# Kernel optimization log

Hardware: AMD Instinct MI355X
Metric: run time of the kernel (lower is better)

The kernel has to match this reference:

```python
import jax, jax.numpy as jnp
import numpy as np

C = 512
NUM_GROUPS = 4
EPS = 1e-6


def _conv1x1(W, b, t):
    # 1x1x1 Conv3d == per-position linear over channels
    return jnp.einsum('oc,bcfhw->bofhw', W, t) + b[None, :, None, None, None]


def setup_inputs() -> dict:
    key = jax.random.key(0)
    ks = jax.random.split(key, 11)
    c = C
    x = jax.random.normal(ks[0], (12, c, 48, 48), dtype=jnp.float32)
    p = lambda k: jax.random.normal(k, (c, c), dtype=jnp.float32) * 0.02
    return {
        'x': x,
        'norm_scale': jnp.ones((c,), jnp.float32),
        'norm_bias': jnp.zeros((c,), jnp.float32),
        'q_w': p(ks[1]), 'q_b': jnp.zeros((c,), jnp.float32),
        'k_w': p(ks[2]), 'k_b': jnp.zeros((c,), jnp.float32),
        'v_w': p(ks[3]), 'v_b': jnp.zeros((c,), jnp.float32),
        'proj_w': p(ks[4]), 'proj_b': jnp.zeros((c,), jnp.float32),
    }


def reference(x, norm_scale, norm_bias, q_w, q_b, k_w, k_b, v_w, v_b, proj_w, proj_b):
    b3, c, h, w = x.shape
    b = b3 // 3
    # chunk batch into 3 frames, stack at frame dim -> (b, c, 3, h, w)
    h_ = jnp.stack(jnp.split(x, 3, axis=0), axis=2)
    # GroupNorm(num_groups=4) over (C/G, F, H, W) per group
    g = NUM_GROUPS
    xg = h_.reshape(b, g, c // g, 3, h, w)
    mean = jnp.mean(xg, axis=(2, 3, 4, 5), keepdims=True)
    var = jnp.var(xg, axis=(2, 3, 4, 5), keepdims=True)
    xn = ((xg - mean) * jax.lax.rsqrt(var + EPS)).reshape(b, c, 3, h, w)
    hn = xn * norm_scale[None, :, None, None, None] + norm_bias[None, :, None, None, None]
    q = _conv1x1(q_w, q_b, hn)[:, :, 1:2]          # middle frame only: (b,c,1,h,w)
    skip = q[:, :, 0]                               # (b,c,h,w)
    k = _conv1x1(k_w, k_b, hn)                      # (b,c,3,h,w)
    v = _conv1x1(v_w, v_b, hn)
    n = h * w
    qf = q.reshape(b, c, n)                         # (b,c,n)
    kf = k.reshape(b, c, 3 * n)                     # (b,c,3n)
    vf = v.reshape(b, c, 3 * n)
    scores = jnp.einsum('bcn,bcm->bnm', qf, kf) * (float(c) ** -0.5)
    attn = jax.nn.softmax(scores, axis=2)           # (b,n,3n)
    out = jnp.einsum('bcm,bnm->bcn', vf, attn).reshape(b, c, 1, h, w)
    out = _conv1x1(proj_w, proj_b, out)[:, :, 0]
    return skip + out
```

## Files before the change

### kernel.cpp

```cpp
#include <hip/hip_runtime.h>

typedef unsigned short u16;
typedef unsigned long long u64;
typedef __attribute__((ext_vector_type(8))) short short8;
typedef __attribute__((ext_vector_type(4))) float f32x4;

__device__ __forceinline__ float bf2f(u16 h) {
    union { unsigned int u; float f; } v; v.u = ((unsigned int)h) << 16; return v.f;
}
__device__ __forceinline__ u16 f2bf(float f) {
    union { float f; unsigned int u; } v; v.f = f;
    unsigned int r = v.u + 0x7fffu + ((v.u >> 16) & 1u);
    return (u16)(r >> 16);
}

__device__ __forceinline__ void gload16(const u16* g, u16* l) {
    __builtin_amdgcn_global_load_lds(
        (const __attribute__((address_space(1))) void*)g,
        (__attribute__((address_space(3))) void*)l,
        16, 0, 0);
}

__device__ __forceinline__ float waveSum(float v) {
#pragma unroll
    for (int o = 32; o > 0; o >>= 1) v += __shfl_down(v, o);
    return v;
}
__device__ __forceinline__ float waveMax(float v) {
#pragma unroll
    for (int o = 32; o > 0; o >>= 1) v = fmaxf(v, __shfl_down(v, o));
    return v;
}
__device__ __forceinline__ int waveSumI(int v) {
#pragma unroll
    for (int o = 32; o > 0; o >>= 1) v += __shfl_down(v, o);
    return v;
}

__global__ __launch_bounds__(256) void detect_k(const u16* __restrict__ x, int* __restrict__ flag) {
    __shared__ int cnt[4];
    int c = 0;
    for (int i = threadIdx.x; i < 8192; i += 256) {
        u16 e = x[i * 2];
        int ex = (e >> 7) & 0xFF;
        c += (ex == 0 || (ex >= 100 && ex <= 150)) ? 1 : 0;
    }
    c = waveSumI(c);
    if ((threadIdx.x & 63) == 0) cnt[threadIdx.x >> 6] = c;
    __syncthreads();
    if (threadIdx.x == 0)
        flag[0] = ((cnt[0] + cnt[1] + cnt[2] + cnt[3]) > 4915) ? 1 : 0;
}

__global__ __launch_bounds__(256) void conv_k(const void* __restrict__ src, u16* __restrict__ dst,
                                              int n8, const int* __restrict__ flag) {
    int i = blockIdx.x * 256 + threadIdx.x;
    if (i >= n8) return;
    if (flag[0]) {
        ((int4*)dst)[i] = ((const int4*)src)[i];
    } else {
        const float* f = (const float*)src + (size_t)i * 8;
        union { int4 v4; u16 o[8]; } tv;
#pragma unroll
        for (int j = 0; j < 8; j++) tv.o[j] = f2bf(f[j]);
        ((int4*)dst)[i] = tv.v4;
    }
}

__global__ __launch_bounds__(256) void conv_w4(const void* s0, const void* s1, const void* s2, const void* s3,
                                               u16* __restrict__ dst, const int* __restrict__ flag) {
    int i = blockIdx.x * 256 + threadIdx.x;
    int w = blockIdx.y;
    const void* s = w == 0 ? s0 : w == 1 ? s1 : w == 2 ? s2 : s3;
    u16* d = dst + (size_t)w * 262144;
    if (flag[0]) {
        ((int4*)d)[i] = ((const int4*)s)[i];
    } else {
        const float* f = (const float*)s + (size_t)i * 8;
        union { int4 v4; u16 o[8]; } tv;
#pragma unroll
        for (int j = 0; j < 8; j++) tv.o[j] = f2bf(f[j]);
        ((int4*)d)[i] = tv.v4;
    }
}

__global__ __launch_bounds__(256) void conv_v6(const void* s0, const void* s1, const void* s2,
                                               const void* s3, const void* s4, const void* s5,
                                               u16* __restrict__ dst, const int* __restrict__ flag) {
    for (int i = threadIdx.x; i < 384; i += 256) {
        int seg = i >> 6, off = i & 63;
        const void* s = seg == 0 ? s0 : seg == 1 ? s1 : seg == 2 ? s2 : seg == 3 ? s3 : seg == 4 ? s4 : s5;
        u16* d = dst + (size_t)seg * 512;
        if (flag[0]) {
            ((int4*)d)[off] = ((const int4*)s)[off];
        } else {
            const float* f = (const float*)s + (size_t)off * 8;
            union { int4 v4; u16 o[8]; } tv;
#pragma unroll
            for (int j = 0; j < 8; j++) tv.o[j] = f2bf(f[j]);
            ((int4*)d)[off] = tv.v4;
        }
    }
}

__global__ __launch_bounds__(256) void gn_stats(const u16* __restrict__ x, float* __restrict__ stat) {
    __shared__ float red[8];
    const int gg = blockIdx.y, chunk = blockIdx.x;
    const int b = gg >> 2, g = gg & 3;
    float s = 0.f, s2 = 0.f;
    for (int pp = 0; pp < 12; pp++) {
        int p = chunk * 12 + pp;
        int t = p >> 7, cc = p & 127;
        const u16* rowp = x + (size_t)((t * 4 + b) * 512 + g * 128 + cc) * 2304;
        for (int vi = threadIdx.x; vi < 288; vi += 256) {
            union { int4 v4; u16 u[8]; } tv;
            tv.v4 = *(const int4*)(rowp + vi * 8);
#pragma unroll
            for (int j = 0; j < 8; j++) { float f = bf2f(tv.u[j]); s += f; s2 += f * f; }
        }
    }
    s = waveSum(s); s2 = waveSum(s2);
    int wid = threadIdx.x >> 6;
    if ((threadIdx.x & 63) == 0) { red[wid] = s; red[wid + 4] = s2; }
    __syncthreads();
    if (threadIdx.x == 0) {
        atomicAdd(&stat[gg], red[0] + red[1] + red[2] + red[3]);
        atomicAdd(&stat[16 + gg], red[4] + red[5] + red[6] + red[7]);
    }
}

__global__ void gn_ab(const float* __restrict__ stat, const u16* __restrict__ scale,
                      const u16* __restrict__ bias, float2* __restrict__ ab) {
    int idx = blockIdx.x * 256 + threadIdx.x;
    int b = idx >> 9, c = idx & 511, g = c >> 7, gg = b * 4 + g;
    const float invN = 1.f / 884736.f;
    float mean = stat[gg] * invN;
    float var  = stat[16 + gg] * invN - mean * mean;
    float rstd = rsqrtf(var + 1e-6f);
    float a = rstd * bf2f(scale[c]);
    ab[idx] = make_float2(a, bf2f(bias[c]) - mean * a);
}

__global__ __launch_bounds__(256) void normT_k(const u16* __restrict__ xb,
                                               const float2* __restrict__ ab,
                                               u16* __restrict__ xnT) {
    __shared__ u16 t[64][72];
    const int zz = blockIdx.z;
    const int b = zz & 3, tt = zz >> 2;
    const u16* s = xb + (size_t)zz * 512 * 2304;
    u16* d = xnT + (size_t)b * (512L * 6912) + (size_t)tt * 2304 * 512;
    const int c0 = blockIdx.x * 64;
    const int r0 = blockIdx.y * 64;
    const int tid = threadIdx.x;
#pragma unroll
    for (int p = 0; p < 4; p++) {
        int r = p * 16 + (tid >> 4);
        int c4 = (tid & 15) * 4;
        float2 sab = ab[b * 512 + r0 + r];
        union { u64 u; u16 e[4]; } tv;
        tv.u = *(const u64*)(s + (size_t)(r0 + r) * 2304 + c0 + c4);
#pragma unroll
        for (int j = 0; j < 4; j++) t[r][c4 + j] = f2bf(bf2f(tv.e[j]) * sab.x + sab.y);
    }
    __syncthreads();
#pragma unroll
    for (int p = 0; p < 2; p++) {
        int n = p * 32 + (tid >> 3);
        int c8 = (tid & 7) * 8;
        union { int4 v4; u16 o[8]; } tv;
#pragma unroll
        for (int j = 0; j < 8; j++) tv.o[j] = t[c8 + j][n];
        *(int4*)(d + (size_t)(c0 + n) * 512 + r0 + c8) = tv.v4;
    }
}

__global__ __launch_bounds__(256) void reduce6(const float* __restrict__ part, u16* __restrict__ outT) {
    const long QS = 1179648;
    size_t idx = ((size_t)blockIdx.x * 256 + threadIdx.x) * 8;
    float s[8] = {0.f, 0.f, 0.f, 0.f, 0.f, 0.f, 0.f, 0.f};
#pragma unroll
    for (int q = 0; q < 6; q++) {
        float4 lo = *(const float4*)(part + q * QS + idx);
        float4 hi = *(const float4*)(part + q * QS + idx + 4);
        s[0] += lo.x; s[1] += lo.y; s[2] += lo.z; s[3] += lo.w;
        s[4] += hi.x; s[5] += hi.y; s[6] += hi.z; s[7] += hi.w;
    }
    union { int4 v4; u16 o[8]; } tv;
#pragma unroll
    for (int j = 0; j < 8; j++) tv.o[j] = f2bf(s[j]);
    *(int4*)(outT + idx) = tv.v4;
}

template<int WR, int WC, int TI, int TJ, int AMODE, int BMODE, int EPI, int F32OUT, int SPLITK, int SWZ>
__global__ __launch_bounds__(256)
void gemm_k(const u16* __restrict__ A, const u16* __restrict__ B, void* __restrict__ Cv,
            const u16* __restrict__ bias, const u16* __restrict__ skip,
            const float2* __restrict__ ab,
            int lda, int ldb, int ldc,
            int K, float alpha, int m_off, int b0,
            long aZS, long bZS, long cZS, long sZS) {
    constexpr int BM = WR * TI * 16;
    constexpr int BN = WC * TJ * 16;
    constexpr int LDA_S = (AMODE == 0) ? 32 : 44;
    constexpr int LDB_S = (BMODE == 1) ? 32 : 44;
    __shared__ alignas(16) u16 As[BM][LDA_S];
    __shared__ alignas(16) u16 Bs[BN][LDB_S];

    int bxi = blockIdx.x, byi = blockIdx.y, bzi = blockIdx.z;
    if (SWZ) {
        int gx = gridDim.x, gy = gridDim.y;
        long NN = (long)gx * gy * gridDim.z;
        long L = bxi + (long)gx * (byi + (long)gy * bzi);
        long q = NN >> 3, r = NN & 7;
        long xc = L & 7, m = L >> 3;
        long nl = (xc < r ? xc * (q + 1) : r * (q + 1) + (xc - r) * q) + m;
        bxi = (int)(nl % gx);
        long t2 = nl / gx;
        byi = (int)(t2 % gy);
        bzi = (int)(t2 / gy);
    }

    const int tid = threadIdx.x;
    const int z = bzi;
    const int i0b = byi * BM;
    const int j0b = bxi * BN;
    const int kstart = SPLITK ? z * K : 0;

    const u16* Ap = A + (size_t)z * aZS;
    const u16* Bp;
    const float2* abp = nullptr;
    int yx0 = 0;
    if (BMODE == 2) {
        int b = b0 + (SPLITK ? 0 : z);
        int m_tile = j0b + m_off;
        int t = m_tile / 2304;
        yx0 = m_tile - t * 2304;
        Bp = B + (size_t)((t * 4 + b) * 512) * 2304;
        abp = ab + b * 512;
    } else {
        Bp = B + (size_t)z * bZS;
    }
    const u16* Sp = (EPI & 10) ? (skip + (size_t)z * sZS) : nullptr;
    float* Cf = (float*)Cv + (size_t)z * (F32OUT ? cZS : 0);
    u16*   Ch = (u16*)Cv   + (size_t)z * (F32OUT ? 0 : cZS);

    const int wave = tid >> 6;
    const int lane = tid & 63;
    const int wr = wave / WC;
    const int wc = wave % WC;
    const int lrow = lane & 15;
    const int quad = lane >> 4;
    const int sws = ((quad ^ ((lrow >> 1) & 3)) << 3);

    f32x4 acc[TI][TJ] = {};

    for (int k0 = kstart; k0 < kstart + K; k0 += 32) {
        __syncthreads();
        if (AMODE == 0) {
            constexpr int NV = (BM * 32 / 8) / 256;
#pragma unroll
            for (int v = 0; v < NV; v++) {
                int vid = tid + v * 256;
                int i = vid >> 2;
                int ks = (((vid & 3) ^ ((vid >> 3) & 3)) * 8);
                gload16(Ap + (size_t)(i0b + i) * lda + (k0 + ks), &As[i][(vid & 3) * 8]);
            }
        } else {
            constexpr int NV = (BM * 32 / 8) / 256;
            constexpr int IG = BM / 8;
#pragma unroll
            for (int v = 0; v < NV; v++) {
                int vid = tid + v * 256;
                int k = vid / IG, ib = (vid % IG) * 8;
                union { int4 v4; u16 s[8]; } tv;
                tv.v4 = *(const int4*)(Ap + (size_t)(k0 + k) * lda + (i0b + ib));
#pragma unroll
                for (int j = 0; j < 8; j++) As[ib + j][k] = tv.s[j];
            }
        }
        if (BMODE == 1) {
            constexpr int NV = (BN * 32 / 8) / 256;
#pragma unroll
            for (int v = 0; v < NV; v++) {
                int vid = tid + v * 256;
                int j = vid >> 2;
                int ks = (((vid & 3) ^ ((vid >> 3) & 3)) * 8);
                gload16(Bp + (size_t)(j0b + j) * ldb + (k0 + ks), &Bs[j][(vid & 3) * 8]);
            }
        } else {
            constexpr int NV = (BN * 32 / 8) / 256;
            constexpr int JG = BN / 8;
#pragma unroll
            for (int v = 0; v < NV; v++) {
                int vid = tid + v * 256;
                int k = vid / JG, jb = (vid % JG) * 8;
                if (BMODE == 0) {
                    union { int4 v4; u16 s[8]; } tv;
                    tv.v4 = *(const int4*)(Bp + (size_t)(k0 + k) * ldb + (j0b + jb));
#pragma unroll
                    for (int j = 0; j < 8; j++) Bs[jb + j][k] = tv.s[j];
                } else {
                    union { int4 v4; u16 s[8]; } tv;
                    tv.v4 = *(const int4*)(Bp + (size_t)(k0 + k) * 2304 + (yx0 + jb));
                    float2 amb = abp[k0 + k];
#pragma unroll
                    for (int j = 0; j < 8; j++)
                        Bs[jb + j][k] = f2bf(bf2f(tv.s[j]) * amb.x + amb.y);
                }
            }
        }
        __syncthreads();
        union FragU { short8 v; u64 u[2]; int4 v4; };
        FragU fa[TI], fb[TJ];
#pragma unroll
        for (int ri = 0; ri < TI; ri++) {
            int r = wr * TI * 16 + ri * 16 + lrow;
            if constexpr (LDA_S == 32) {
                fa[ri].v4 = *(const int4*)(&As[r][sws]);
            } else {
                fa[ri].u[0] = *(const u64*)(&As[r][quad * 8]);
                fa[ri].u[1] = *(const u64*)(&As[r][quad * 8 + 4]);
            }
        }
#pragma unroll
        for (int cj = 0; cj < TJ; cj++) {
            int cc2 = wc * TJ * 16 + cj * 16 + lrow;
            if constexpr (LDB_S == 32) {
                fb[cj].v4 = *(const int4*)(&Bs[cc2][sws]);
            } else {
                fb[cj].u[0] = *(const u64*)(&Bs[cc2][quad * 8]);
                fb[cj].u[1] = *(const u64*)(&Bs[cc2][quad * 8 + 4]);
            }
        }
#pragma unroll
        for (int ri = 0; ri < TI; ri++)
#pragma unroll
            for (int cj = 0; cj < TJ; cj++)
                acc[ri][cj] = __builtin_amdgcn_mfma_f32_16x16x32_bf16(
                    fa[ri].v, fb[cj].v, acc[ri][cj], 0, 0, 0);
    }

#pragma unroll
    for (int ri = 0; ri < TI; ri++) {
#pragma unroll
        for (int reg = 0; reg < 4; reg++) {
            int gi = i0b + wr * TI * 16 + ri * 16 + quad * 4 + reg;
            float bv = (EPI & 1) ? bf2f(bias[gi]) : 0.f;
#pragma unroll
            for (int cj = 0; cj < TJ; cj++) {
                int gj = j0b + wc * TJ * 16 + cj * 16 + lrow;
                float v = acc[ri][cj][reg] * alpha + bv;
                if (EPI & 4) v += bf2f(bias[gj]);
                if (EPI & 2) v += bf2f(Sp[(size_t)gi * ldc + gj]);
                if (EPI & 8) v += bf2f(Sp[(size_t)gj * 512 + gi]);
                if (F32OUT) Cf[(size_t)gi * ldc + gj] = v;
                else        Ch[(size_t)gi * ldc + gj] = f2bf(v);
            }
        }
    }
}

__global__ __launch_bounds__(256) void softmax_k(u16* __restrict__ sb, long zs) {
    __shared__ float row[6912];
    __shared__ float red[8];
    u16* p = sb + (size_t)blockIdx.y * zs + (size_t)blockIdx.x * 6912;
    const int tid = threadIdx.x;
    float mx = -3.0e38f;
    for (int vi = tid; vi < 864; vi += 256) {
        union { int4 v4; u16 u[8]; } tv;
        tv.v4 = *(const int4*)(p + vi * 8);
#pragma unroll
        for (int j = 0; j < 8; j++) { float f = bf2f(tv.u[j]); row[vi * 8 + j] = f; mx = fmaxf(mx, f); }
    }
    mx = waveMax(mx);
    if ((tid & 63) == 0) red[tid >> 6] = mx;
    __syncthreads();
    mx = fmaxf(fmaxf(red[0], red[1]), fmaxf(red[2], red[3]));
    __syncthreads();
    float sum = 0.f;
    for (int i = tid; i < 6912; i += 256) {
        float e = __expf(row[i] - mx);
        row[i] = e; sum += e;
    }
    sum = waveSum(sum);
    if ((tid & 63) == 0) red[4 + (tid >> 6)] = sum;
    __syncthreads();
    float inv = 1.f / (red[4] + red[5] + red[6] + red[7]);
    for (int vi = tid; vi < 864; vi += 256) {
        union { int4 v4; u16 u[8]; } tv;
#pragma unroll
        for (int j = 0; j < 8; j++) tv.u[j] = f2bf(row[vi * 8 + j] * inv);
        *(int4*)(p + vi * 8) = tv.v4;
    }
}

extern "C" void kernel_launch(void* const* d_in, const int* in_sizes, int n_in,
                              void* d_out, int out_size, void* d_ws, size_t ws_size,
                              hipStream_t stream) {
    float* out = (float*)d_out;

    const long QS = (long)512 * 2304;
    const long KS = (long)512 * 6912;
    const long SS = (long)2304 * 6912;
    const long PS = (long)512 * 2304;
    const float rs = 0.044194173824159216f;

    const size_t FIXED = 256 + 256 + 2048 * sizeof(float2)
                       + (size_t)14155776 * 2 + (size_t)4 * 262144 * 2 + 8192
                       + (size_t)14155776 * 2;
    const size_t PERNB = (size_t)(QS + KS + KS + QS + SS) * 2;
    int nb = 0;
    if      (ws_size >= FIXED + 4 * PERNB) nb = 4;
    else if (ws_size >= FIXED + 2 * PERNB) nb = 2;
    else if (ws_size >= FIXED + 1 * PERNB) nb = 1;

    char* w = (char*)d_ws;
    int*    flag = (int*)w;     w += 256;
    float*  stat = (float*)w;   w += 256;
    float2* ab   = (float2*)w;  w += 2048 * sizeof(float2);
    u16* xb = (u16*)w;  w += (size_t)14155776 * 2;
    u16* wgt = (u16*)w; w += (size_t)4 * 262144 * 2;
    u16* vecb = (u16*)w; w += 8192;

    detect_k<<<1, 256, 0, stream>>>((const u16*)d_in[0], flag);
    conv_k<<<6912, 256, 0, stream>>>(d_in[0], xb, 1769472, flag);
    conv_w4<<<dim3(128, 4), 256, 0, stream>>>(d_in[3], d_in[5], d_in[7], d_in[9], wgt, flag);
    conv_v6<<<1, 256, 0, stream>>>(d_in[1], d_in[2], d_in[4], d_in[6], d_in[8], d_in[10], vecb, flag);
    hipMemsetAsync(stat, 0, 32 * sizeof(float), stream);
    gn_stats<<<dim3(32, 16), 256, 0, stream>>>(xb, stat);
    gn_ab<<<8, 256, 0, stream>>>(stat, vecb, vecb + 512, ab);

    const u16* qw = wgt;
    const u16* kw = wgt + 262144;
    const u16* vw = wgt + 2 * 262144;
    const u16* pw = wgt + 3 * 262144;
    const u16* qb2 = vecb + 1024, *kb2 = vecb + 1536, *vb2 = vecb + 2048, *pb2 = vecb + 2560;

    if (nb == 0) {
        u16* qbuf = (u16*)w;  w += QS * 2;
        u16* kbuf = (u16*)w;  w += KS * 2;
        u16* vbuf = (u16*)w;  w += KS * 2;
        u16* obuf = (u16*)w;  w += QS * 2;
        u16* sbuf = (u16*)w;
        for (int b = 0; b < 4; b++) {
            gemm_k<2,2,4,4,0,2,1,0,0,0><<<dim3(54,4,1),256,0,stream>>>(
                kw, xb, kbuf, kb2, nullptr, ab, 512,0,6912, 512,1.f,0,b, 0,0,0,0);
            gemm_k<2,2,4,4,0,2,1,0,0,0><<<dim3(54,4,1),256,0,stream>>>(
                vw, xb, vbuf, vb2, nullptr, ab, 512,0,6912, 512,1.f,0,b, 0,0,0,0);
            gemm_k<2,2,4,4,0,2,1,0,0,0><<<dim3(18,4,1),256,0,stream>>>(
                qw, xb, qbuf, qb2, nullptr, ab, 512,0,2304, 512,1.f,2304,b, 0,0,0,0);
            gemm_k<2,2,4,4,1,0,0,0,0,0><<<dim3(54,18,1),256,0,stream>>>(
                qbuf, kbuf, sbuf, nullptr,nullptr,nullptr, 2304,6912,6912, 512,rs,0,b, 0,0,0,0);
            softmax_k<<<dim3(2304,1),256,0,stream>>>(sbuf, 0);
            gemm_k<1,4,4,1,0,1,0,0,0,0><<<dim3(36,8,1),256,0,stream>>>(
                vbuf, sbuf, obuf, nullptr,nullptr,nullptr, 6912,6912,2304, 6912,1.f,0,b, 0,0,0,0);
            gemm_k<2,2,4,2,0,0,3,1,0,0><<<dim3(36,4,1),256,0,stream>>>(
                pw, obuf, out + (size_t)b * PS, pb2, qbuf, nullptr,
                512,2304,2304, 512,1.f,0,b, 0,0,0,0);
        }
        return;
    }

    u16* xnT = (u16*)w; w += (size_t)14155776 * 2;
    u16* qT  = (u16*)w; w += (size_t)nb * QS * 2;
    u16* kT  = (u16*)w; w += (size_t)nb * KS * 2;
    u16* vbuf= (u16*)w; w += (size_t)nb * KS * 2;
    u16* obT = (u16*)w; w += (size_t)nb * QS * 2;
    u16* sbuf= (u16*)w; w += (size_t)nb * SS * 2;
    float* opart = (float*)xb;

    normT_k<<<dim3(36, 8, 12), 256, 0, stream>>>(xb, ab, xnT);

    for (int g = 0; g < 4; g += nb) {
        gemm_k<2,2,4,4,0,1,4,0,0,1><<<dim3(4,54,nb),256,0,stream>>>(
            xnT + (size_t)g * KS, kw, kT, kb2, nullptr, nullptr,
            512,512,512, 512,1.f,0,g, KS,0,KS,0);
        gemm_k<2,2,4,4,0,1,4,0,0,1><<<dim3(4,18,nb),256,0,stream>>>(
            xnT + (size_t)g * KS + (size_t)2304 * 512, qw, qT, qb2, nullptr, nullptr,
            512,512,512, 512,1.f,0,g, KS,0,QS,0);
        gemm_k<2,2,4,4,0,1,1,0,0,1><<<dim3(54,4,nb),256,0,stream>>>(
            vw, xnT + (size_t)g * KS, vbuf, vb2, nullptr, nullptr,
            512,512,6912, 512,1.f,0,g, 0,KS,KS,0);
        gemm_k<2,2,4,4,0,1,0,0,0,1><<<dim3(54,18,nb),256,0,stream>>>(
            qT, kT, sbuf, nullptr,nullptr,nullptr, 512,512,6912, 512,rs,0,g, QS,KS,SS,0);
        softmax_k<<<dim3(2304,nb),256,0,stream>>>(sbuf, SS);
        for (int bb = 0; bb < nb; bb++) {
            gemm_k<2,2,4,4,0,1,0,1,1,1><<<dim3(4,18,6),256,0,stream>>>(
                sbuf + (size_t)bb * SS, vbuf + (size_t)bb * KS, opart,
                nullptr,nullptr,nullptr, 6912,6912,512, 1152,1.f,0,0, 0,0,QS,0);
            reduce6<<<576,256,0,stream>>>(opart, obT + (size_t)bb * QS);
        }
        gemm_k<2,2,4,2,0,1,9,1,0,1><<<dim3(36,4,nb),256,0,stream>>>(
            pw, obT, out + (size_t)g * PS, pb2, qT, nullptr,
            512,512,2304, 512,1.f,0,g, 0,QS,PS,QS);
    }
}
```

Baseline: 544.3 us.

## Double-buffer GEMM shared-memory tiles and replace split-K PV with direct batched GEMM

Every GEMM instance now keeps two shared-memory tile buffers, so the next K-slice is staged while MFMAs run on the current one, with one barrier per iteration instead of two. The attention-output GEMM (scores times V) no longer uses six-way split-K with fp32 partials and a separate reduce kernel. It becomes a single batched launch with smaller M tiles (TI=2) that writes bf16 output directly. This removes the partial-sum traffic and extra launches, at the cost of doubled LDS per block, which may lower occupancy, and fewer blocks for the long-K GEMM.

```diff
diff --git a/kernel.cpp b/kernel.cpp
--- a/kernel.cpp
+++ b/kernel.cpp
@@ -174,23 +174,6 @@
     }
 }
 
-__global__ __launch_bounds__(256) void reduce6(const float* __restrict__ part, u16* __restrict__ outT) {
-    const long QS = 1179648;
-    size_t idx = ((size_t)blockIdx.x * 256 + threadIdx.x) * 8;
-    float s[8] = {0.f, 0.f, 0.f, 0.f, 0.f, 0.f, 0.f, 0.f};
-#pragma unroll
-    for (int q = 0; q < 6; q++) {
-        float4 lo = *(const float4*)(part + q * QS + idx);
-        float4 hi = *(const float4*)(part + q * QS + idx + 4);
-        s[0] += lo.x; s[1] += lo.y; s[2] += lo.z; s[3] += lo.w;
-        s[4] += hi.x; s[5] += hi.y; s[6] += hi.z; s[7] += hi.w;
-    }
-    union { int4 v4; u16 o[8]; } tv;
-#pragma unroll
-    for (int j = 0; j < 8; j++) tv.o[j] = f2bf(s[j]);
-    *(int4*)(outT + idx) = tv.v4;
-}
-
 template<int WR, int WC, int TI, int TJ, int AMODE, int BMODE, int EPI, int F32OUT, int SPLITK, int SWZ>
 __global__ __launch_bounds__(256)
 void gemm_k(const u16* __restrict__ A, const u16* __restrict__ B, void* __restrict__ Cv,
@@ -203,8 +186,8 @@
     constexpr int BN = WC * TJ * 16;
     constexpr int LDA_S = (AMODE == 0) ? 32 : 44;
     constexpr int LDB_S = (BMODE == 1) ? 32 : 44;
-    __shared__ alignas(16) u16 As[BM][LDA_S];
-    __shared__ alignas(16) u16 Bs[BN][LDB_S];
+    __shared__ alignas(16) u16 As[2][BM][LDA_S];
+    __shared__ alignas(16) u16 Bs[2][BN][LDB_S];
 
     int bxi = blockIdx.x, byi = blockIdx.y, bzi = blockIdx.z;
     if (SWZ) {
@@ -252,10 +235,7 @@
     const int quad = lane >> 4;
     const int sws = ((quad ^ ((lrow >> 1) & 3)) << 3);
 
-    f32x4 acc[TI][TJ] = {};
-
-    for (int k0 = kstart; k0 < kstart + K; k0 += 32) {
-        __syncthreads();
+    auto stage = [&](int bsel, int k0) {
         if (AMODE == 0) {
             constexpr int NV = (BM * 32 / 8) / 256;
 #pragma unroll
@@ -263,7 +243,7 @@
                 int vid = tid + v * 256;
                 int i = vid >> 2;
                 int ks = (((vid & 3) ^ ((vid >> 3) & 3)) * 8);
-                gload16(Ap + (size_t)(i0b + i) * lda + (k0 + ks), &As[i][(vid & 3) * 8]);
+                gload16(Ap + (size_t)(i0b + i) * lda + (k0 + ks), &As[bsel][i][(vid & 3) * 8]);
             }
         } else {
             constexpr int NV = (BM * 32 / 8) / 256;
@@ -275,7 +255,7 @@
                 union { int4 v4; u16 s[8]; } tv;
                 tv.v4 = *(const int4*)(Ap + (size_t)(k0 + k) * lda + (i0b + ib));
 #pragma unroll
-                for (int j = 0; j < 8; j++) As[ib + j][k] = tv.s[j];
+                for (int j = 0; j < 8; j++) As[bsel][ib + j][k] = tv.s[j];
             }
         }
         if (BMODE == 1) {
@@ -285,7 +265,7 @@
                 int vid = tid + v * 256;
                 int j = vid >> 2;
                 int ks = (((vid & 3) ^ ((vid >> 3) & 3)) * 8);
-                gload16(Bp + (size_t)(j0b + j) * ldb + (k0 + ks), &Bs[j][(vid & 3) * 8]);
+                gload16(Bp + (size_t)(j0b + j) * ldb + (k0 + ks), &Bs[bsel][j][(vid & 3) * 8]);
             }
         } else {
             constexpr int NV = (BN * 32 / 8) / 256;
@@ -298,38 +278,49 @@
                     union { int4 v4; u16 s[8]; } tv;
                     tv.v4 = *(const int4*)(Bp + (size_t)(k0 + k) * ldb + (j0b + jb));
 #pragma unroll
-                    for (int j = 0; j < 8; j++) Bs[jb + j][k] = tv.s[j];
+                    for (int j = 0; j < 8; j++) Bs[bsel][jb + j][k] = tv.s[j];
                 } else {
                     union { int4 v4; u16 s[8]; } tv;
                     tv.v4 = *(const int4*)(Bp + (size_t)(k0 + k) * 2304 + (yx0 + jb));
                     float2 amb = abp[k0 + k];
 #pragma unroll
                     for (int j = 0; j < 8; j++)
-                        Bs[jb + j][k] = f2bf(bf2f(tv.s[j]) * amb.x + amb.y);
+                        Bs[bsel][jb + j][k] = f2bf(bf2f(tv.s[j]) * amb.x + amb.y);
                 }
             }
         }
-        __syncthreads();
+    };
+
+    f32x4 acc[TI][TJ] = {};
+    const int kend = kstart + K;
+
+    stage(0, kstart);
+    __syncthreads();
+
+    int cur = 0;
+    for (int k0 = kstart; k0 < kend; k0 += 32) {
+        if (k0 + 32 < kend) stage(cur ^ 1, k0 + 32);
+
         union FragU { short8 v; u64 u[2]; int4 v4; };
         FragU fa[TI], fb[TJ];
 #pragma unroll
         for (int ri = 0; ri < TI; ri++) {
             int r = wr * TI * 16 + ri * 16 + lrow;
             if constexpr (LDA_S == 32) {
-                fa[ri].v4 = *(const int4*)(&As[r][sws]);
+                fa[ri].v4 = *(const int4*)(&As[cur][r][sws]);
             } else {
-                fa[ri].u[0] = *(const u64*)(&As[r][quad * 8]);
-                fa[ri].u[1] = *(const u64*)(&As[r][quad * 8 + 4]);
+                fa[ri].u[0] = *(const u64*)(&As[cur][r][quad * 8]);
+                fa[ri].u[1] = *(const u64*)(&As[cur][r][quad * 8 + 4]);
             }
         }
 #pragma unroll
         for (int cj = 0; cj < TJ; cj++) {
             int cc2 = wc * TJ * 16 + cj * 16 + lrow;
             if constexpr (LDB_S == 32) {
-                fb[cj].v4 = *(const int4*)(&Bs[cc2][sws]);
+                fb[cj].v4 = *(const int4*)(&Bs[cur][cc2][sws]);
             } else {
-                fb[cj].u[0] = *(const u64*)(&Bs[cc2][quad * 8]);
-                fb[cj].u[1] = *(const u64*)(&Bs[cc2][quad * 8 + 4]);
+                fb[cj].u[0] = *(const u64*)(&Bs[cur][cc2][quad * 8]);
+                fb[cj].u[1] = *(const u64*)(&Bs[cur][cc2][quad * 8 + 4]);
             }
         }
 #pragma unroll
@@ -338,6 +329,9 @@
             for (int cj = 0; cj < TJ; cj++)
                 acc[ri][cj] = __builtin_amdgcn_mfma_f32_16x16x32_bf16(
                     fa[ri].v, fb[cj].v, acc[ri][cj], 0, 0, 0);
+
+        __syncthreads();
+        cur ^= 1;
     }
 
 #pragma unroll
@@ -467,7 +461,6 @@
     u16* vbuf= (u16*)w; w += (size_t)nb * KS * 2;
     u16* obT = (u16*)w; w += (size_t)nb * QS * 2;
     u16* sbuf= (u16*)w; w += (size_t)nb * SS * 2;
-    float* opart = (float*)xb;
 
     normT_k<<<dim3(36, 8, 12), 256, 0, stream>>>(xb, ab, xnT);
 
@@ -484,12 +477,8 @@
         gemm_k<2,2,4,4,0,1,0,0,0,1><<<dim3(54,18,nb),256,0,stream>>>(
             qT, kT, sbuf, nullptr,nullptr,nullptr, 512,512,6912, 512,rs,0,g, QS,KS,SS,0);
         softmax_k<<<dim3(2304,nb),256,0,stream>>>(sbuf, SS);
-        for (int bb = 0; bb < nb; bb++) {
-            gemm_k<2,2,4,4,0,1,0,1,1,1><<<dim3(4,18,6),256,0,stream>>>(
-                sbuf + (size_t)bb * SS, vbuf + (size_t)bb * KS, opart,
-                nullptr,nullptr,nullptr, 6912,6912,512, 1152,1.f,0,0, 0,0,QS,0);
-            reduce6<<<576,256,0,stream>>>(opart, obT + (size_t)bb * QS);
-        }
+        gemm_k<2,2,2,4,0,1,0,0,0,1><<<dim3(4,36,nb),256,0,stream>>>(
+            sbuf, vbuf, obT, nullptr,nullptr,nullptr, 6912,6912,512, 6912,1.f,0,g, SS,KS,QS,0);
         gemm_k<2,2,4,2,0,1,9,1,0,1><<<dim3(36,4,nb),256,0,stream>>>(
             pw, obT, out + (size_t)g * PS, pb2, qT, nullptr,
             512,512,2304, 512,1.f,0,g, 0,QS,PS,QS);
```

New measurement: 502.3 us. 7.7% less time.
